# Performance work log

Measured on AMD Instinct MI355X. Metric: run time of the kernel, lower is better.

Reference implementation:

```python
import jax, jax.numpy as jnp
import numpy as np

NUM_GRAPHS = 512


def setup_inputs() -> dict:
    key = jax.random.key(0)
    ks = jax.random.split(key, 16)
    N, E = 50000, 800000
    x = jax.random.normal(ks[0], (N, 3), dtype=jnp.float32)
    edge_index = jax.random.randint(ks[1], (2, E), 0, N, dtype=jnp.int64)
    batch = jnp.sort(jax.random.randint(ks[2], (N,), 0, NUM_GRAPHS, dtype=jnp.int64))

    def glorot(k, shape):
        fan_in, fan_out = shape
        lim = (6.0 / (fan_in + fan_out)) ** 0.5
        return jax.random.uniform(k, shape, jnp.float32, -lim, lim)

    return {
        "x": x, "edge_index": edge_index, "batch": batch,
        "W1": glorot(ks[3], (3, 32)),   "b1": jnp.zeros((32,), jnp.float32),
        "W2": glorot(ks[4], (32, 64)),  "b2": jnp.zeros((64,), jnp.float32),
        "W3": glorot(ks[5], (64, 128)), "b3": jnp.zeros((128,), jnp.float32),
        "Wf1": glorot(ks[6], (128, 32)), "bf1": jnp.zeros((32,), jnp.float32),
        "Wf2": glorot(ks[7], (32, 4)),   "bf2": jnp.zeros((4,), jnp.float32),
    }


def _gcn_conv(x, src, dst, norm, W, b, N):
    # GCNConv: h = x W, then symmetric-normalized aggregation, then bias.
    h = x @ W                                   # [N, out]
    msg = h[src] * norm[:, None]                # [E+N, out] gathered edge messages
    out = jax.ops.segment_sum(msg, dst, num_segments=N)
    return out + b


def reference(x, edge_index, batch, W1, b1, W2, b2, W3, b3, Wf1, bf1, Wf2, bf2):
    N = x.shape[0]
    loops = jnp.arange(N, dtype=edge_index.dtype)
    src = jnp.concatenate([edge_index[0], loops])   # add self-loops (GCNConv default)
    dst = jnp.concatenate([edge_index[1], loops])
    # symmetric normalization deg^-1/2[src] * deg^-1/2[dst], deg counted on dst
    deg = jax.ops.segment_sum(jnp.ones_like(dst, dtype=x.dtype), dst, num_segments=N)
    dinv = jnp.where(deg > 0, jax.lax.rsqrt(deg), 0.0)
    norm = dinv[src] * dinv[dst]                    # [E+N]

    h = jax.nn.relu(_gcn_conv(x, src, dst, norm, W1, b1, N))
    h = jax.nn.relu(_gcn_conv(h, src, dst, norm, W2, b2, N))
    h = jax.nn.relu(_gcn_conv(h, src, dst, norm, W3, b3, N))

    # global mean pool over graphs
    sums = jax.ops.segment_sum(h, batch, num_segments=NUM_GRAPHS)
    cnts = jax.ops.segment_sum(jnp.ones((N,), h.dtype), batch, num_segments=NUM_GRAPHS)
    pooled = sums / jnp.maximum(cnts, 1.0)[:, None]   # [G, 128]

    z = jax.nn.relu(pooled @ Wf1 + bf1)
    return z @ Wf2 + bf2                              # [G, 4]
```

## Files before the change

### kernel.cpp

```cpp
#include <hip/hip_runtime.h>

#define NN 50000
#define NE 800000
#define NG 512
#define CAP 64
#define NP 196
#define CH 3200
#define NCH 250

__global__ __launch_bounds__(256) void p1_hist_k(const int* __restrict__ dst,
                                                 int* __restrict__ Ht, int e) {
    __shared__ int lh[NP];
    int t = threadIdx.x, b = blockIdx.x;
    if (t < NP) lh[t] = 0;
    __syncthreads();
    int i0 = b * CH, i1 = min(e, i0 + CH);
    for (int i = i0 + t; i < i1; i += 256) atomicAdd(&lh[dst[i] >> 8], 1);
    __syncthreads();
    if (t < NP) Ht[t * NCH + b] = lh[t];
}

__global__ __launch_bounds__(256) void p2a_k(int* __restrict__ Ht, int* __restrict__ tot) {
    __shared__ int sh[256];
    int p = blockIdx.x, t = threadIdx.x;
    int v = (t < NCH) ? Ht[p * NCH + t] : 0;
    sh[t] = v;
    __syncthreads();
    for (int off = 1; off < 256; off <<= 1) {
        int x = (t >= off) ? sh[t - off] : 0;
        __syncthreads();
        sh[t] += x;
        __syncthreads();
    }
    if (t < NCH) Ht[p * NCH + t] = sh[t] - v;
    if (t == 255) tot[p] = sh[255];
}

__global__ __launch_bounds__(256) void p2b_k(const int* __restrict__ tot,
                                             int* __restrict__ start) {
    __shared__ int sh[256];
    int t = threadIdx.x;
    int v = (t < NP) ? tot[t] : 0;
    sh[t] = v;
    __syncthreads();
    for (int off = 1; off < 256; off <<= 1) {
        int x = (t >= off) ? sh[t - off] : 0;
        __syncthreads();
        sh[t] += x;
        __syncthreads();
    }
    if (t < NP) start[t] = sh[t] - v;
    if (t == 255) start[NP] = sh[255];
}

__global__ __launch_bounds__(256) void p3_place_k(const int* __restrict__ src,
                                                  const int* __restrict__ dst,
                                                  const int* __restrict__ Ht,
                                                  const int* __restrict__ start,
                                                  int* __restrict__ pak, int e) {
    __shared__ int cur[NP];
    int t = threadIdx.x, b = blockIdx.x;
    if (t < NP) cur[t] = start[t] + Ht[t * NCH + b];
    __syncthreads();
    int i0 = b * CH, i1 = min(e, i0 + CH);
    for (int i = i0 + t; i < i1; i += 256) {
        int d = dst[i], s = src[i];
        int p = d >> 8, dl = d & 255;
        int pos = atomicAdd(&cur[p], 1);
        pak[pos] = s | (dl << 16);
    }
}

__global__ __launch_bounds__(256) void p4_build_k(const int* __restrict__ pak,
                                                  const int* __restrict__ start,
                                                  const float* __restrict__ x,
                                                  int* __restrict__ fill,
                                                  float* __restrict__ dinv,
                                                  float* __restrict__ xs,
                                                  int* __restrict__ eidx, int n) {
    __shared__ int lh[256], curn[256];
    int p = blockIdx.x, t = threadIdx.x;
    lh[t] = 0;
    curn[t] = 0;
    __syncthreads();
    int s0 = start[p], s1 = start[p + 1];
    for (int i = s0 + t; i < s1; i += 256) atomicAdd(&lh[pak[i] >> 16], 1);
    __syncthreads();
    int node = p * 256 + t;
    if (node < n) {
        int dg = lh[t];
        fill[node] = dg;
        float d = rsqrtf((float)(dg + 1));
        dinv[node] = d;
        float4 v;
        v.x = x[node * 3 + 0] * d;
        v.y = x[node * 3 + 1] * d;
        v.z = x[node * 3 + 2] * d;
        v.w = 0.0f;
        *(float4*)(xs + (size_t)node * 4) = v;
    }
    __syncthreads();
    for (int i = s0 + t; i < s1; i += 256) {
        int w = pak[i];
        int dl = w >> 16, s = w & 0xFFFF;
        int pos = atomicAdd(&curn[dl], 1) & (CAP - 1);
        eidx[(size_t)(p * 256 + dl) * CAP + pos] = s;
    }
}

__global__ __launch_bounds__(256) void fused_l1_k(
    const int* __restrict__ deg, const int* __restrict__ eidx,
    const float* __restrict__ xs, const float* __restrict__ W1,
    const float* __restrict__ b1, const float* __restrict__ dinv,
    float* __restrict__ A2, int n) {
    __shared__ float act[64][4];
    int t = threadIdx.x;
    int node0 = blockIdx.x * 64;
    {
        int node = node0 + (t >> 2);
        int f = t & 3;
        if (node < n) {
            int e1 = deg[node];
            const int* __restrict__ eb = eidx + node * CAP;
            float acc = xs[(size_t)node * 4 + f];
            int e = 0;
            for (; e + 4 <= e1; e += 4) {
                int4 s = *(const int4*)(eb + e);
                float v0 = xs[(size_t)s.x * 4 + f];
                float v1 = xs[(size_t)s.y * 4 + f];
                float v2 = xs[(size_t)s.z * 4 + f];
                float v3 = xs[(size_t)s.w * 4 + f];
                acc += (v0 + v1) + (v2 + v3);
            }
            for (; e < e1; ++e) acc += xs[(size_t)eb[e] * 4 + f];
            act[t >> 2][f] = acc;
        }
    }
    __syncthreads();
    int f = t & 31;
    int nl0 = t >> 5;
#pragma unroll
    for (int i = 0; i < 8; ++i) {
        int nl = nl0 + i * 8;
        int node = node0 + nl;
        if (node < n) {
            float acc = act[nl][0] * W1[f] + act[nl][1] * W1[32 + f] + act[nl][2] * W1[64 + f];
            float s = dinv[node];
            A2[(size_t)node * 32 + f] = fmaxf(fmaf(s, acc, b1[f]), 0.0f) * s;
        }
    }
}

template <int F>
__global__ __launch_bounds__(256) void gather4_k(const int* __restrict__ deg,
                                                 const int* __restrict__ eidx,
                                                 const float* __restrict__ A,
                                                 float* __restrict__ B, int n) {
    constexpr int FV = F / 4;
    constexpr int NPB = 256 / FV;
    int t = threadIdx.x;
    int node = blockIdx.x * NPB + t / FV;
    int j = (t % FV) * 4;
    if (node >= n) return;
    int e1 = deg[node];
    const int* __restrict__ eb = eidx + node * CAP;
    const float* __restrict__ Aj = A + j;
    float4 a0 = *(const float4*)(Aj + (size_t)node * F);
    float4 a1 = make_float4(0.f, 0.f, 0.f, 0.f);
    float4 a2 = make_float4(0.f, 0.f, 0.f, 0.f);
    float4 a3 = make_float4(0.f, 0.f, 0.f, 0.f);
    int e = 0;
    for (; e + 16 <= e1; e += 16) {
        int4 sa = *(const int4*)(eb + e);
        int4 sb = *(const int4*)(eb + e + 4);
        int4 sc = *(const int4*)(eb + e + 8);
        int4 sd = *(const int4*)(eb + e + 12);
        float4 v0 = *(const float4*)(Aj + (size_t)sa.x * F);
        float4 v1 = *(const float4*)(Aj + (size_t)sa.y * F);
        float4 v2 = *(const float4*)(Aj + (size_t)sa.z * F);
        float4 v3 = *(const float4*)(Aj + (size_t)sa.w * F);
        float4 v4 = *(const float4*)(Aj + (size_t)sb.x * F);
        float4 v5 = *(const float4*)(Aj + (size_t)sb.y * F);
        float4 v6 = *(const float4*)(Aj + (size_t)sb.z * F);
        float4 v7 = *(const float4*)(Aj + (size_t)sb.w * F);
        float4 v8 = *(const float4*)(Aj + (size_t)sc.x * F);
        float4 v9 = *(const float4*)(Aj + (size_t)sc.y * F);
        float4 va = *(const float4*)(Aj + (size_t)sc.z * F);
        float4 vb = *(const float4*)(Aj + (size_t)sc.w * F);
        float4 vc = *(const float4*)(Aj + (size_t)sd.x * F);
        float4 vd = *(const float4*)(Aj + (size_t)sd.y * F);
        float4 ve = *(const float4*)(Aj + (size_t)sd.z * F);
        float4 vf = *(const float4*)(Aj + (size_t)sd.w * F);
        a0.x += (v0.x + v1.x) + (v2.x + v3.x);
        a0.y += (v0.y + v1.y) + (v2.y + v3.y);
        a0.z += (v0.z + v1.z) + (v2.z + v3.z);
        a0.w += (v0.w + v1.w) + (v2.w + v3.w);
        a1.x += (v4.x + v5.x) + (v6.x + v7.x);
        a1.y += (v4.y + v5.y) + (v6.y + v7.y);
        a1.z += (v4.z + v5.z) + (v6.z + v7.z);
        a1.w += (v4.w + v5.w) + (v6.w + v7.w);
        a2.x += (v8.x + v9.x) + (va.x + vb.x);
        a2.y += (v8.y + v9.y) + (va.y + vb.y);
        a2.z += (v8.z + v9.z) + (va.z + vb.z);
        a2.w += (v8.w + v9.w) + (va.w + vb.w);
        a3.x += (vc.x + vd.x) + (ve.x + vf.x);
        a3.y += (vc.y + vd.y) + (ve.y + vf.y);
        a3.z += (vc.z + vd.z) + (ve.z + vf.z);
        a3.w += (vc.w + vd.w) + (ve.w + vf.w);
    }
    for (; e + 4 <= e1; e += 4) {
        int4 sa = *(const int4*)(eb + e);
        float4 v0 = *(const float4*)(Aj + (size_t)sa.x * F);
        float4 v1 = *(const float4*)(Aj + (size_t)sa.y * F);
        float4 v2 = *(const float4*)(Aj + (size_t)sa.z * F);
        float4 v3 = *(const float4*)(Aj + (size_t)sa.w * F);
        a1.x += (v0.x + v1.x) + (v2.x + v3.x);
        a1.y += (v0.y + v1.y) + (v2.y + v3.y);
        a1.z += (v0.z + v1.z) + (v2.z + v3.z);
        a1.w += (v0.w + v1.w) + (v2.w + v3.w);
    }
    for (; e < e1; ++e) {
        float4 v = *(const float4*)(Aj + (size_t)eb[e] * F);
        a0.x += v.x; a0.y += v.y; a0.z += v.z; a0.w += v.w;
    }
    a0.x += (a1.x + a2.x) + a3.x;
    a0.y += (a1.y + a2.y) + a3.y;
    a0.z += (a1.z + a2.z) + a3.z;
    a0.w += (a1.w + a2.w) + a3.w;
    *(float4*)(B + (size_t)node * F + j) = a0;
}

template <int F>
__global__ __launch_bounds__(256) void gatherbf_k(const int* __restrict__ deg,
                                                  const int* __restrict__ eidx,
                                                  const float* __restrict__ Aself,
                                                  const uint4* __restrict__ Ab,
                                                  float* __restrict__ B, int n) {
    constexpr int FV = F / 8;
    constexpr int NPB = 256 / FV;
    constexpr int RU4 = F / 8;
    int t = threadIdx.x;
    int node = blockIdx.x * NPB + t / FV;
    int j = (t % FV) * 8;
    if (node >= n) return;
    int e1 = deg[node];
    const int* __restrict__ eb = eidx + (size_t)node * CAP;
    const uint4* __restrict__ Aj = Ab + (j >> 3);
    float4 p0 = *(const float4*)(Aself + (size_t)node * F + j);
    float4 p1 = *(const float4*)(Aself + (size_t)node * F + j + 4);
    float4 q0 = make_float4(0.f, 0.f, 0.f, 0.f);
    float4 q1 = make_float4(0.f, 0.f, 0.f, 0.f);
#define BF_UNPACK8(u, lo, hi)                                                 \
    {                                                                         \
        lo.x += __uint_as_float((u).x << 16);                                 \
        lo.y += __uint_as_float((u).x & 0xFFFF0000u);                         \
        lo.z += __uint_as_float((u).y << 16);                                 \
        lo.w += __uint_as_float((u).y & 0xFFFF0000u);                         \
        hi.x += __uint_as_float((u).z << 16);                                 \
        hi.y += __uint_as_float((u).z & 0xFFFF0000u);                         \
        hi.z += __uint_as_float((u).w << 16);                                 \
        hi.w += __uint_as_float((u).w & 0xFFFF0000u);                         \
    }
    int e = 0;
    for (; e + 16 <= e1; e += 16) {
        int4 sa = *(const int4*)(eb + e);
        int4 sb = *(const int4*)(eb + e + 4);
        int4 sc = *(const int4*)(eb + e + 8);
        int4 sd = *(const int4*)(eb + e + 12);
        uint4 v0 = Aj[(size_t)sa.x * RU4];
        uint4 v1 = Aj[(size_t)sa.y * RU4];
        uint4 v2 = Aj[(size_t)sa.z * RU4];
        uint4 v3 = Aj[(size_t)sa.w * RU4];
        uint4 v4 = Aj[(size_t)sb.x * RU4];
        uint4 v5 = Aj[(size_t)sb.y * RU4];
        uint4 v6 = Aj[(size_t)sb.z * RU4];
        uint4 v7 = Aj[(size_t)sb.w * RU4];
        uint4 v8 = Aj[(size_t)sc.x * RU4];
        uint4 v9 = Aj[(size_t)sc.y * RU4];
        uint4 va = Aj[(size_t)sc.z * RU4];
        uint4 vb = Aj[(size_t)sc.w * RU4];
        uint4 vc = Aj[(size_t)sd.x * RU4];
        uint4 vd = Aj[(size_t)sd.y * RU4];
        uint4 ve = Aj[(size_t)sd.z * RU4];
        uint4 vf = Aj[(size_t)sd.w * RU4];
        BF_UNPACK8(v0, p0, p1) BF_UNPACK8(v1, q0, q1)
        BF_UNPACK8(v2, p0, p1) BF_UNPACK8(v3, q0, q1)
        BF_UNPACK8(v4, p0, p1) BF_UNPACK8(v5, q0, q1)
        BF_UNPACK8(v6, p0, p1) BF_UNPACK8(v7, q0, q1)
        BF_UNPACK8(v8, p0, p1) BF_UNPACK8(v9, q0, q1)
        BF_UNPACK8(va, p0, p1) BF_UNPACK8(vb, q0, q1)
        BF_UNPACK8(vc, p0, p1) BF_UNPACK8(vd, q0, q1)
        BF_UNPACK8(ve, p0, p1) BF_UNPACK8(vf, q0, q1)
    }
    for (; e + 4 <= e1; e += 4) {
        int4 sa = *(const int4*)(eb + e);
        uint4 v0 = Aj[(size_t)sa.x * RU4];
        uint4 v1 = Aj[(size_t)sa.y * RU4];
        uint4 v2 = Aj[(size_t)sa.z * RU4];
        uint4 v3 = Aj[(size_t)sa.w * RU4];
        BF_UNPACK8(v0, p0, p1) BF_UNPACK8(v1, q0, q1)
        BF_UNPACK8(v2, p0, p1) BF_UNPACK8(v3, q0, q1)
    }
    for (; e < e1; ++e) {
        uint4 v = Aj[(size_t)eb[e] * RU4];
        BF_UNPACK8(v, p0, p1)
    }
#undef BF_UNPACK8
    p0.x += q0.x; p0.y += q0.y; p0.z += q0.z; p0.w += q0.w;
    p1.x += q1.x; p1.y += q1.y; p1.z += q1.z; p1.w += q1.w;
    *(float4*)(B + (size_t)node * F + j) = p0;
    *(float4*)(B + (size_t)node * F + j + 4) = p1;
}

__device__ __forceinline__ unsigned short f2bf_rn(float f) {
    unsigned int u = __float_as_uint(f);
    u += 0x7FFFu + ((u >> 16) & 1u);
    return (unsigned short)(u >> 16);
}

template <int Fin, int Fout, int NPB, bool SCALE_OUT, bool WRITE_BF>
__global__ __launch_bounds__(256) void mmB_k(
    const float* __restrict__ G, const float* __restrict__ W,
    const float* __restrict__ bias, const float* __restrict__ dinv,
    float* __restrict__ Aout, unsigned short* __restrict__ Abf, int n) {
    constexpr int FL = Fout / 4;
    constexpr int NGRP = 256 / FL;
    constexpr int NPT = NPB / NGRP;
    __shared__ float act[NPB][Fin];
    int t = threadIdx.x;
    int node0 = blockIdx.x * NPB;
    constexpr int TOT4 = NPB * Fin / 4;
    const float4* __restrict__ G4 = (const float4*)(G + (size_t)node0 * Fin);
    float4* act4 = (float4*)&act[0][0];
    for (int i = t; i < TOT4; i += 256) {
        int nl = i / (Fin / 4);
        float4 v = make_float4(0.f, 0.f, 0.f, 0.f);
        if (node0 + nl < n) v = G4[i];
        act4[i] = v;
    }
    __syncthreads();
    int f4 = (t % FL) * 4;
    int nlbase = (t / FL) * NPT;
    float4 acc[NPT];
#pragma unroll
    for (int i = 0; i < NPT; ++i) acc[i] = make_float4(0.f, 0.f, 0.f, 0.f);
    for (int k = 0; k < Fin; k += 4) {
        float4 a[NPT];
#pragma unroll
        for (int i = 0; i < NPT; ++i) a[i] = *(const float4*)&act[nlbase + i][k];
#pragma unroll
        for (int kk = 0; kk < 4; ++kk) {
            float4 w = *(const float4*)(W + (size_t)(k + kk) * Fout + f4);
#pragma unroll
            for (int i = 0; i < NPT; ++i) {
                float av = (&a[i].x)[kk];
                acc[i].x = fmaf(av, w.x, acc[i].x);
                acc[i].y = fmaf(av, w.y, acc[i].y);
                acc[i].z = fmaf(av, w.z, acc[i].z);
                acc[i].w = fmaf(av, w.w, acc[i].w);
            }
        }
    }
    float4 bv = *(const float4*)(bias + f4);
#pragma unroll
    for (int i = 0; i < NPT; ++i) {
        int node = node0 + nlbase + i;
        if (node < n) {
            float s = dinv[node];
            float4 o;
            o.x = fmaxf(fmaf(s, acc[i].x, bv.x), 0.0f);
            o.y = fmaxf(fmaf(s, acc[i].y, bv.y), 0.0f);
            o.z = fmaxf(fmaf(s, acc[i].z, bv.z), 0.0f);
            o.w = fmaxf(fmaf(s, acc[i].w, bv.w), 0.0f);
            if (SCALE_OUT) { o.x *= s; o.y *= s; o.z *= s; o.w *= s; }
            *(float4*)(Aout + (size_t)node * Fout + f4) = o;
            if (WRITE_BF) {
                ushort4 ob;
                ob.x = f2bf_rn(o.x); ob.y = f2bf_rn(o.y);
                ob.z = f2bf_rn(o.z); ob.w = f2bf_rn(o.w);
                *(ushort4*)(Abf + (size_t)node * Fout + f4) = ob;
            }
        }
    }
}

__device__ __forceinline__ int lbound_d(const int* __restrict__ a, int n, int key) {
    int lo = 0, hi = n;
    while (lo < hi) {
        int m = (lo + hi) >> 1;
        if (a[m] < key) lo = m + 1; else hi = m;
    }
    return lo;
}

__global__ __launch_bounds__(128) void poolhead_k(
    const float* __restrict__ H, const int* __restrict__ batch,
    const float* __restrict__ Wf1, const float* __restrict__ bf1,
    const float* __restrict__ Wf2, const float* __restrict__ bf2,
    float* __restrict__ out, int n) {
    __shared__ int bnd[2];
    __shared__ float pm[128];
    __shared__ float z[32];
    int g = blockIdx.x, t = threadIdx.x;
    if (t == 0) bnd[0] = lbound_d(batch, n, g);
    if (t == 1) bnd[1] = lbound_d(batch, n, g + 1);
    __syncthreads();
    int lo = bnd[0], hi = bnd[1];
    float s0 = 0.f, s1 = 0.f, s2 = 0.f, s3 = 0.f;
    int i = lo;
    for (; i + 4 <= hi; i += 4) {
        s0 += H[(size_t)i * 128 + t];
        s1 += H[(size_t)(i + 1) * 128 + t];
        s2 += H[(size_t)(i + 2) * 128 + t];
        s3 += H[(size_t)(i + 3) * 128 + t];
    }
    for (; i < hi; ++i) s0 += H[(size_t)i * 128 + t];
    float c = (float)(hi - lo);
    c = fmaxf(c, 1.0f);
    pm[t] = ((s0 + s1) + (s2 + s3)) / c;
    __syncthreads();
    if (t < 32) {
        float acc = bf1[t];
#pragma unroll 4
        for (int k = 0; k < 128; ++k) acc = fmaf(pm[k], Wf1[k * 32 + t], acc);
        z[t] = fmaxf(acc, 0.0f);
    }
    __syncthreads();
    if (t < 4) {
        float acc = bf2[t];
#pragma unroll
        for (int jj = 0; jj < 32; ++jj) acc = fmaf(z[jj], Wf2[jj * 4 + t], acc);
        out[g * 4 + t] = acc;
    }
}

extern "C" void kernel_launch(void* const* d_in, const int* in_sizes, int n_in,
                              void* d_out, int out_size, void* d_ws, size_t ws_size,
                              hipStream_t stream) {
    const float* x    = (const float*)d_in[0];
    const int*   ei   = (const int*)d_in[1];
    const int*   batch= (const int*)d_in[2];
    const float* W1   = (const float*)d_in[3];
    const float* b1   = (const float*)d_in[4];
    const float* W2   = (const float*)d_in[5];
    const float* b2   = (const float*)d_in[6];
    const float* W3   = (const float*)d_in[7];
    const float* b3   = (const float*)d_in[8];
    const float* Wf1  = (const float*)d_in[9];
    const float* bf1  = (const float*)d_in[10];
    const float* Wf2  = (const float*)d_in[11];
    const float* bf2  = (const float*)d_in[12];
    float* out = (float*)d_out;

    int*   fill   = (int*)d_ws;
    float* dinv   = (float*)(fill + NN);
    float* xs     = dinv + NN;
    float* A2     = xs + (size_t)NN * 4;
    float* A3     = A2 + (size_t)NN * 32;
    float* H3     = A3 + (size_t)NN * 64;
    float* G      = H3 + (size_t)NN * 128;
    int*   eidx   = (int*)(G + (size_t)NN * 64);
    unsigned short* A3b = (unsigned short*)(eidx + (size_t)NN * CAP);

    int* pak   = (int*)G;
    int* Ht    = (int*)H3;
    int* tot   = Ht + NP * NCH;
    int* start = tot + 256;

    const int* src = ei;
    const int* dst = ei + NE;

    p1_hist_k<<<NCH, 256, 0, stream>>>(dst, Ht, NE);
    p2a_k<<<NP, 256, 0, stream>>>(Ht, tot);
    p2b_k<<<1, 256, 0, stream>>>(tot, start);
    p3_place_k<<<NCH, 256, 0, stream>>>(src, dst, Ht, start, pak, NE);
    p4_build_k<<<NP, 256, 0, stream>>>(pak, start, x, fill, dinv, xs, eidx, NN);

    fused_l1_k<<<(NN + 63) / 64, 256, 0, stream>>>(fill, eidx, xs, W1, b1, dinv, A2, NN);

    gather4_k<32><<<(NN + 31) / 32, 256, 0, stream>>>(fill, eidx, A2, G, NN);
    mmB_k<32, 64, 32, true, true><<<(NN + 31) / 32, 256, 0, stream>>>(
        G, W2, b2, dinv, A3, A3b, NN);

    gatherbf_k<64><<<(NN + 31) / 32, 256, 0, stream>>>(
        fill, eidx, A3, (const uint4*)A3b, G, NN);
    mmB_k<64, 128, 32, false, false><<<(NN + 31) / 32, 256, 0, stream>>>(
        G, W3, b3, dinv, H3, (unsigned short*)nullptr, NN);

    poolhead_k<<<NG, 128, 0, stream>>>(H3, batch, Wf1, bf1, Wf2, bf2, out, NN);
}
```

Baseline: 213.1 us.

## Fuse layer-3 matmul with mean pooling and use bf16 gather for layer 2

The layer-3 dense transform now accumulates per-graph sums directly in shared memory and atomically adds them into a global pooled buffer, so the full N×128 activation is no longer written and re-read by the pooling kernel. The layer-1 kernel also writes a bf16 copy of its output and zeroes the pooled buffer, and layer-2 aggregation switches to the bf16 gather kernel to halve the bytes gathered per edge. The costs are floating-point atomics, which make summation order nondeterministic, and extra bf16 rounding error in the layer-2 inputs.

```diff
diff --git a/kernel.cpp b/kernel.cpp
--- a/kernel.cpp
+++ b/kernel.cpp
@@ -108,13 +108,21 @@
     }
 }
 
+__device__ __forceinline__ unsigned short f2bf_rn(float f) {
+    unsigned int u = __float_as_uint(f);
+    u += 0x7FFFu + ((u >> 16) & 1u);
+    return (unsigned short)(u >> 16);
+}
+
 __global__ __launch_bounds__(256) void fused_l1_k(
     const int* __restrict__ deg, const int* __restrict__ eidx,
     const float* __restrict__ xs, const float* __restrict__ W1,
     const float* __restrict__ b1, const float* __restrict__ dinv,
-    float* __restrict__ A2, int n) {
+    float* __restrict__ A2, unsigned short* __restrict__ A2b,
+    float* __restrict__ pooled, int n) {
     __shared__ float act[64][4];
     int t = threadIdx.x;
+    if (blockIdx.x < 256) pooled[blockIdx.x * 256 + t] = 0.0f;
     int node0 = blockIdx.x * 64;
     {
         int node = node0 + (t >> 2);
@@ -146,88 +154,11 @@
         if (node < n) {
             float acc = act[nl][0] * W1[f] + act[nl][1] * W1[32 + f] + act[nl][2] * W1[64 + f];
             float s = dinv[node];
-            A2[(size_t)node * 32 + f] = fmaxf(fmaf(s, acc, b1[f]), 0.0f) * s;
-        }
-    }
-}
-
-template <int F>
-__global__ __launch_bounds__(256) void gather4_k(const int* __restrict__ deg,
-                                                 const int* __restrict__ eidx,
-                                                 const float* __restrict__ A,
-                                                 float* __restrict__ B, int n) {
-    constexpr int FV = F / 4;
-    constexpr int NPB = 256 / FV;
-    int t = threadIdx.x;
-    int node = blockIdx.x * NPB + t / FV;
-    int j = (t % FV) * 4;
-    if (node >= n) return;
-    int e1 = deg[node];
-    const int* __restrict__ eb = eidx + node * CAP;
-    const float* __restrict__ Aj = A + j;
-    float4 a0 = *(const float4*)(Aj + (size_t)node * F);
-    float4 a1 = make_float4(0.f, 0.f, 0.f, 0.f);
-    float4 a2 = make_float4(0.f, 0.f, 0.f, 0.f);
-    float4 a3 = make_float4(0.f, 0.f, 0.f, 0.f);
-    int e = 0;
-    for (; e + 16 <= e1; e += 16) {
-        int4 sa = *(const int4*)(eb + e);
-        int4 sb = *(const int4*)(eb + e + 4);
-        int4 sc = *(const int4*)(eb + e + 8);
-        int4 sd = *(const int4*)(eb + e + 12);
-        float4 v0 = *(const float4*)(Aj + (size_t)sa.x * F);
-        float4 v1 = *(const float4*)(Aj + (size_t)sa.y * F);
-        float4 v2 = *(const float4*)(Aj + (size_t)sa.z * F);
-        float4 v3 = *(const float4*)(Aj + (size_t)sa.w * F);
-        float4 v4 = *(const float4*)(Aj + (size_t)sb.x * F);
-        float4 v5 = *(const float4*)(Aj + (size_t)sb.y * F);
-        float4 v6 = *(const float4*)(Aj + (size_t)sb.z * F);
-        float4 v7 = *(const float4*)(Aj + (size_t)sb.w * F);
-        float4 v8 = *(const float4*)(Aj + (size_t)sc.x * F);
-        float4 v9 = *(const float4*)(Aj + (size_t)sc.y * F);
-        float4 va = *(const float4*)(Aj + (size_t)sc.z * F);
-        float4 vb = *(const float4*)(Aj + (size_t)sc.w * F);
-        float4 vc = *(const float4*)(Aj + (size_t)sd.x * F);
-        float4 vd = *(const float4*)(Aj + (size_t)sd.y * F);
-        float4 ve = *(const float4*)(Aj + (size_t)sd.z * F);
-        float4 vf = *(const float4*)(Aj + (size_t)sd.w * F);
-        a0.x += (v0.x + v1.x) + (v2.x + v3.x);
-        a0.y += (v0.y + v1.y) + (v2.y + v3.y);
-        a0.z += (v0.z + v1.z) + (v2.z + v3.z);
-        a0.w += (v0.w + v1.w) + (v2.w + v3.w);
-        a1.x += (v4.x + v5.x) + (v6.x + v7.x);
-        a1.y += (v4.y + v5.y) + (v6.y + v7.y);
-        a1.z += (v4.z + v5.z) + (v6.z + v7.z);
-        a1.w += (v4.w + v5.w) + (v6.w + v7.w);
-        a2.x += (v8.x + v9.x) + (va.x + vb.x);
-        a2.y += (v8.y + v9.y) + (va.y + vb.y);
-        a2.z += (v8.z + v9.z) + (va.z + vb.z);
-        a2.w += (v8.w + v9.w) + (va.w + vb.w);
-        a3.x += (vc.x + vd.x) + (ve.x + vf.x);
-        a3.y += (vc.y + vd.y) + (ve.y + vf.y);
-        a3.z += (vc.z + vd.z) + (ve.z + vf.z);
-        a3.w += (vc.w + vd.w) + (ve.w + vf.w);
-    }
-    for (; e + 4 <= e1; e += 4) {
-        int4 sa = *(const int4*)(eb + e);
-        float4 v0 = *(const float4*)(Aj + (size_t)sa.x * F);
-        float4 v1 = *(const float4*)(Aj + (size_t)sa.y * F);
-        float4 v2 = *(const float4*)(Aj + (size_t)sa.z * F);
-        float4 v3 = *(const float4*)(Aj + (size_t)sa.w * F);
-        a1.x += (v0.x + v1.x) + (v2.x + v3.x);
-        a1.y += (v0.y + v1.y) + (v2.y + v3.y);
-        a1.z += (v0.z + v1.z) + (v2.z + v3.z);
-        a1.w += (v0.w + v1.w) + (v2.w + v3.w);
-    }
-    for (; e < e1; ++e) {
-        float4 v = *(const float4*)(Aj + (size_t)eb[e] * F);
-        a0.x += v.x; a0.y += v.y; a0.z += v.z; a0.w += v.w;
-    }
-    a0.x += (a1.x + a2.x) + a3.x;
-    a0.y += (a1.y + a2.y) + a3.y;
-    a0.z += (a1.z + a2.z) + a3.z;
-    a0.w += (a1.w + a2.w) + a3.w;
-    *(float4*)(B + (size_t)node * F + j) = a0;
+            float o = fmaxf(fmaf(s, acc, b1[f]), 0.0f) * s;
+            A2[(size_t)node * 32 + f] = o;
+            A2b[(size_t)node * 32 + f] = f2bf_rn(o);
+        }
+    }
 }
 
 template <int F>
@@ -312,12 +243,6 @@
     *(float4*)(B + (size_t)node * F + j + 4) = p1;
 }
 
-__device__ __forceinline__ unsigned short f2bf_rn(float f) {
-    unsigned int u = __float_as_uint(f);
-    u += 0x7FFFu + ((u >> 16) & 1u);
-    return (unsigned short)(u >> 16);
-}
-
 template <int Fin, int Fout, int NPB, bool SCALE_OUT, bool WRITE_BF>
 __global__ __launch_bounds__(256) void mmB_k(
     const float* __restrict__ G, const float* __restrict__ W,
@@ -384,6 +309,83 @@
     }
 }
 
+__global__ __launch_bounds__(256) void mm3_pool_k(
+    const float* __restrict__ G, const float* __restrict__ W,
+    const float* __restrict__ bias, const float* __restrict__ dinv,
+    const int* __restrict__ batch, float* __restrict__ pooled, int n) {
+    constexpr int Fin = 64, Fout = 128, NPB = 32;
+    constexpr int FL = Fout / 4;
+    constexpr int NPT = NPB / (256 / FL);
+    __shared__ float act[NPB][Fin];
+    __shared__ float pool[NPB][Fout];
+    int t = threadIdx.x;
+    int node0 = blockIdx.x * NPB;
+    {
+        float4* p4 = (float4*)&pool[0][0];
+        for (int i = t; i < NPB * Fout / 4; i += 256) p4[i] = make_float4(0.f, 0.f, 0.f, 0.f);
+    }
+    constexpr int TOT4 = NPB * Fin / 4;
+    const float4* __restrict__ G4 = (const float4*)(G + (size_t)node0 * Fin);
+    float4* act4 = (float4*)&act[0][0];
+    for (int i = t; i < TOT4; i += 256) {
+        int nl = i / (Fin / 4);
+        float4 v = make_float4(0.f, 0.f, 0.f, 0.f);
+        if (node0 + nl < n) v = G4[i];
+        act4[i] = v;
+    }
+    __syncthreads();
+    int f4 = (t % FL) * 4;
+    int nlbase = (t / FL) * NPT;
+    float4 acc[NPT];
+#pragma unroll
+    for (int i = 0; i < NPT; ++i) acc[i] = make_float4(0.f, 0.f, 0.f, 0.f);
+    for (int k = 0; k < Fin; k += 4) {
+        float4 a[NPT];
+#pragma unroll
+        for (int i = 0; i < NPT; ++i) a[i] = *(const float4*)&act[nlbase + i][k];
+#pragma unroll
+        for (int kk = 0; kk < 4; ++kk) {
+            float4 w = *(const float4*)(W + (size_t)(k + kk) * Fout + f4);
+#pragma unroll
+            for (int i = 0; i < NPT; ++i) {
+                float av = (&a[i].x)[kk];
+                acc[i].x = fmaf(av, w.x, acc[i].x);
+                acc[i].y = fmaf(av, w.y, acc[i].y);
+                acc[i].z = fmaf(av, w.z, acc[i].z);
+                acc[i].w = fmaf(av, w.w, acc[i].w);
+            }
+        }
+    }
+    int g0 = batch[node0 < n ? node0 : (n - 1)];
+    float4 bv = *(const float4*)(bias + f4);
+#pragma unroll
+    for (int i = 0; i < NPT; ++i) {
+        int node = node0 + nlbase + i;
+        if (node < n) {
+            float s = dinv[node];
+            float4 o;
+            o.x = fmaxf(fmaf(s, acc[i].x, bv.x), 0.0f);
+            o.y = fmaxf(fmaf(s, acc[i].y, bv.y), 0.0f);
+            o.z = fmaxf(fmaf(s, acc[i].z, bv.z), 0.0f);
+            o.w = fmaxf(fmaf(s, acc[i].w, bv.w), 0.0f);
+            int gl = batch[node] - g0;
+            atomicAdd(&pool[gl][f4 + 0], o.x);
+            atomicAdd(&pool[gl][f4 + 1], o.y);
+            atomicAdd(&pool[gl][f4 + 2], o.z);
+            atomicAdd(&pool[gl][f4 + 3], o.w);
+        }
+    }
+    __syncthreads();
+    int lastn = min(node0 + NPB - 1, n - 1);
+    int g1 = batch[lastn];
+    int ng = g1 - g0 + 1;
+    for (int i = t; i < ng * Fout; i += 256) {
+        int gl = i >> 7, ff = i & 127;
+        float v = pool[gl][ff];
+        if (v != 0.0f) atomicAdd(&pooled[(size_t)(g0 + gl) * Fout + ff], v);
+    }
+}
+
 __device__ __forceinline__ int lbound_d(const int* __restrict__ a, int n, int key) {
     int lo = 0, hi = n;
     while (lo < hi) {
@@ -393,8 +395,8 @@
     return lo;
 }
 
-__global__ __launch_bounds__(128) void poolhead_k(
-    const float* __restrict__ H, const int* __restrict__ batch,
+__global__ __launch_bounds__(128) void head_k(
+    const float* __restrict__ pooled, const int* __restrict__ batch,
     const float* __restrict__ Wf1, const float* __restrict__ bf1,
     const float* __restrict__ Wf2, const float* __restrict__ bf2,
     float* __restrict__ out, int n) {
@@ -402,22 +404,10 @@
     __shared__ float pm[128];
     __shared__ float z[32];
     int g = blockIdx.x, t = threadIdx.x;
-    if (t == 0) bnd[0] = lbound_d(batch, n, g);
-    if (t == 1) bnd[1] = lbound_d(batch, n, g + 1);
-    __syncthreads();
-    int lo = bnd[0], hi = bnd[1];
-    float s0 = 0.f, s1 = 0.f, s2 = 0.f, s3 = 0.f;
-    int i = lo;
-    for (; i + 4 <= hi; i += 4) {
-        s0 += H[(size_t)i * 128 + t];
-        s1 += H[(size_t)(i + 1) * 128 + t];
-        s2 += H[(size_t)(i + 2) * 128 + t];
-        s3 += H[(size_t)(i + 3) * 128 + t];
-    }
-    for (; i < hi; ++i) s0 += H[(size_t)i * 128 + t];
-    float c = (float)(hi - lo);
-    c = fmaxf(c, 1.0f);
-    pm[t] = ((s0 + s1) + (s2 + s3)) / c;
+    if (t < 2) bnd[t] = lbound_d(batch, n, g + t);
+    __syncthreads();
+    float c = fmaxf((float)(bnd[1] - bnd[0]), 1.0f);
+    pm[t] = pooled[(size_t)g * 128 + t] / c;
     __syncthreads();
     if (t < 32) {
         float acc = bf1[t];
@@ -461,6 +451,8 @@
     float* G      = H3 + (size_t)NN * 128;
     int*   eidx   = (int*)(G + (size_t)NN * 64);
     unsigned short* A3b = (unsigned short*)(eidx + (size_t)NN * CAP);
+    unsigned short* A2b = A3b + (size_t)NN * 64;
+    float* pooled = (float*)(A2b + (size_t)NN * 32);
 
     int* pak   = (int*)G;
     int* Ht    = (int*)H3;
@@ -476,16 +468,18 @@
     p3_place_k<<<NCH, 256, 0, stream>>>(src, dst, Ht, start, pak, NE);
     p4_build_k<<<NP, 256, 0, stream>>>(pak, start, x, fill, dinv, xs, eidx, NN);
 
-    fused_l1_k<<<(NN + 63) / 64, 256, 0, stream>>>(fill, eidx, xs, W1, b1, dinv, A2, NN);
-
-    gather4_k<32><<<(NN + 31) / 32, 256, 0, stream>>>(fill, eidx, A2, G, NN);
+    fused_l1_k<<<(NN + 63) / 64, 256, 0, stream>>>(
+        fill, eidx, xs, W1, b1, dinv, A2, A2b, pooled, NN);
+
+    gatherbf_k<32><<<(NN + 63) / 64, 256, 0, stream>>>(
+        fill, eidx, A2, (const uint4*)A2b, G, NN);
     mmB_k<32, 64, 32, true, true><<<(NN + 31) / 32, 256, 0, stream>>>(
         G, W2, b2, dinv, A3, A3b, NN);
 
     gatherbf_k<64><<<(NN + 31) / 32, 256, 0, stream>>>(
         fill, eidx, A3, (const uint4*)A3b, G, NN);
-    mmB_k<64, 128, 32, false, false><<<(NN + 31) / 32, 256, 0, stream>>>(
-        G, W3, b3, dinv, H3, (unsigned short*)nullptr, NN);
-
-    poolhead_k<<<NG, 128, 0, stream>>>(H3, batch, Wf1, bf1, Wf2, bf2, out, NN);
-}
+    mm3_pool_k<<<(NN + 31) / 32, 256, 0, stream>>>(
+        G, W3, b3, dinv, batch, pooled, NN);
+
+    head_k<<<NG, 128, 0, stream>>>(pooled, batch, Wf1, bf1, Wf2, bf2, out, NN);
+}
```

Result: slower. 230.7 us (+8.3%).
